# Kernel tuning notes

Hardware: AMD Instinct MI355X
Metric: run time of the kernel (lower is better)

Reference implementation:

```python
import jax, jax.numpy as jnp
import numpy as np

B, L, D, F = 4096, 200, 64, 100000


def setup_inputs() -> dict:
    key = jax.random.key(0)
    ks = jax.random.split(key, 12)
    film_hist = jax.random.randint(ks[0], (B, L), 0, F)                 # padded rated-film indices
    ratings = jax.random.uniform(ks[1], (B, L), jnp.float32) * 4.5 + 0.5  # letterboxd-style 0.5..5
    lengths = jax.random.randint(ks[2], (B,), 1, L + 1)                 # ragged history lengths (>=1)
    film_indices = jax.random.randint(ks[3], (B,), 0, F)                # target films to score
    emb_table = jax.random.normal(ks[4], (F, D), jnp.float32) * 0.1
    W1 = jax.random.normal(ks[5], (5 * D, 2 * D), jnp.float32) * 0.05
    b1 = jnp.zeros((2 * D,), jnp.float32)
    W2 = jax.random.normal(ks[6], (2 * D, D), jnp.float32) * 0.05
    b2 = jnp.zeros((D,), jnp.float32)
    W3 = jax.random.normal(ks[7], (D, 1), jnp.float32) * 0.05
    b3 = jnp.zeros((1,), jnp.float32)
    return {"film_hist": film_hist, "ratings": ratings, "lengths": lengths,
            "film_indices": film_indices, "emb_table": emb_table,
            "W1": W1, "b1": b1, "W2": W2, "b2": b2, "W3": W3, "b3": b3}


def _user_embeddings(film_hist, ratings, lengths, emb_table):
    # mask[b, l] = l < lengths[b]
    mask = jnp.arange(L)[None, :] < lengths[:, None]          # [B, L]
    n = lengths.astype(jnp.float32)                           # [B]
    mean_r = jnp.sum(jnp.where(mask, ratings, 0.0), axis=1) / n
    weights = ratings - mean_r[:, None] + 0.1                 # [B, L]
    hist_emb = emb_table[film_hist]                           # [B, L, D]
    w = hist_emb * weights[:, :, None]                        # weighted film embeddings
    m3 = mask[:, :, None]
    wmin = jnp.min(jnp.where(m3, w, jnp.inf), axis=1)
    wmax = jnp.max(jnp.where(m3, w, -jnp.inf), axis=1)
    wmean = jnp.sum(jnp.where(m3, w, 0.0), axis=1) / n[:, None]
    # median: sort valid entries (pads go to +inf at the end); torch.median
    # returns the lower middle element -> index (n-1)//2
    ws = jnp.sort(jnp.where(m3, w, jnp.inf), axis=1)
    mid = ((lengths - 1) // 2)[:, None, None]                 # [B,1,1]
    wmed = jnp.take_along_axis(ws, jnp.broadcast_to(mid, (B, 1, D)), axis=1)[:, 0, :]
    ue = jnp.concatenate([wmin, wmax, wmean, wmed], axis=1)   # [B, 4D]
    return ue / jnp.linalg.norm(ue, axis=1, keepdims=True)


def reference(film_hist, ratings, lengths, film_indices, emb_table, W1, b1, W2, b2, W3, b3):
    ue = _user_embeddings(film_hist, ratings, lengths, emb_table)  # [B, 4D]
    fe = emb_table[film_indices]                                   # [B, D]
    x = jnp.concatenate([ue, fe], axis=1)                          # [B, 5D]
    h = jax.nn.relu(x @ W1 + b1)   # Dropout(0.2) is identity in eval
    h = jax.nn.relu(h @ W2 + b2)
    return jax.nn.sigmoid(h @ W3 + b3)[:, 0]                       # [B]
```

## Files before the change

### kernel.cpp

```cpp
#include <hip/hip_runtime.h>
#include <hip/hip_bf16.h>
#include <stdint.h>


#define B_ 4096
#define L_ 200
#define D_ 64
#define LPAD 224

__device__ __forceinline__ void xpose_sign(uint32_t (&W)[16]) {
  #define XS(k, jj, m) { uint32_t tt = ((W[k] ^ (W[(k)|(jj)] >> (jj))) & (m)); \
                         W[k] ^= tt; W[(k)|(jj)] ^= (tt << (jj)); }
  XS(0,8,0x00FF00FFu) XS(1,8,0x00FF00FFu) XS(2,8,0x00FF00FFu) XS(3,8,0x00FF00FFu)
  XS(4,8,0x00FF00FFu) XS(5,8,0x00FF00FFu) XS(6,8,0x00FF00FFu) XS(7,8,0x00FF00FFu)
  XS(0,4,0x0F0F0F0Fu) XS(1,4,0x0F0F0F0Fu) XS(2,4,0x0F0F0F0Fu) XS(3,4,0x0F0F0F0Fu)
  XS(8,4,0x0F0F0F0Fu) XS(9,4,0x0F0F0F0Fu) XS(10,4,0x0F0F0F0Fu) XS(11,4,0x0F0F0F0Fu)
  XS(0,2,0x33333333u) XS(1,2,0x33333333u) XS(4,2,0x33333333u) XS(5,2,0x33333333u)
  XS(8,2,0x33333333u) XS(9,2,0x33333333u) XS(12,2,0x33333333u) XS(13,2,0x33333333u)
  XS(0,1,0x55555555u) XS(2,1,0x55555555u) XS(4,1,0x55555555u) XS(6,1,0x55555555u)
  XS(8,1,0x55555555u) XS(10,1,0x55555555u) XS(12,1,0x55555555u) XS(14,1,0x55555555u)
  #undef XS
  const uint32_t S = W[0];
  W[0] = ~S;
  #pragma unroll
  for (int j = 1; j < 16; ++j) W[j] ^= S;
}

template<bool TWO>
__device__ __forceinline__ uint32_t select_med(
    const uint32_t (&W0)[16], const uint32_t (&W1x)[16],
    uint32_t a0, uint32_t a1, int k)
{
  uint32_t prefix = 0;
  #pragma unroll
  for (int bb = 15; bb >= 0; --bb) {
    const uint32_t z0 = a0 & ~W0[15 - bb];
    int cnt = __popc(z0);
    uint32_t z1 = 0u;
    if (TWO) {
      z1 = a1 & ~W1x[15 - bb];
      cnt += __popc(z1);
    }
    cnt += __builtin_amdgcn_update_dpp(0, cnt, 0xB1, 0xF, 0xF, true);
    cnt += __builtin_amdgcn_update_dpp(0, cnt, 0x4E, 0xF, 0xF, true);
    const bool zs = (k < cnt);
    a0 = zs ? z0 : (a0 ^ z0);
    if (TWO) a1 = zs ? z1 : (a1 ^ z1);
    k      = zs ? k : (k - cnt);
    prefix = zs ? prefix : (prefix | (1u << bb));
  }
  return prefix;
}

__global__ __launch_bounds__(256) void stats_kernel(
    const int* __restrict__ film_hist,
    const float* __restrict__ ratings,
    const int* __restrict__ lengths,
    const int* __restrict__ film_indices,
    const float* __restrict__ emb,
    float* __restrict__ x)
{
  __shared__ uint2 pair_s[LPAD];
  __shared__ float red[4];
  __shared__ float ue[4*D_];

  const int t = threadIdx.x;
  const int wv = t >> 6;
  const int lane = t & 63;
  const int d = t >> 2;
  const int sub = t & 3;
  const int b = blockIdx.x;
  const int n = lengths[b];

  const int fi = film_indices[b];
  const float fev = (t < 64) ? emb[(size_t)fi * D_ + t] : 0.f;

  float r = 0.f;
  if (t < LPAD) {
    uint2 e;
    if (t < n) {
      e.x = ((uint32_t)film_hist[(size_t)b*L_ + t]) << 8;
      r = ratings[(size_t)b*L_ + t];
      e.y = __float_as_uint(r);
    } else {
      e.x = 0u; e.y = 0u;
    }
    pair_s[t] = e;
  }
  float s = r;
  #pragma unroll
  for (int off = 32; off; off >>= 1) s += __shfl_down(s, off);
  if (lane == 0) red[wv] = s;
  __syncthreads();
  const float mr1 = 0.1f - (red[0]+red[1]+red[2]+red[3]) / (float)n;

  if (t < n) pair_s[t].y = __float_as_uint(r + mr1);
  __syncthreads();

  const char* eb = (const char*)emb;
  const uint32_t d4 = (uint32_t)d * 4u;
  float vmin = __builtin_inff(), vmax = -__builtin_inff(), vsum = 0.f;
  uint32_t W0[16], W1x[16];
  #pragma unroll
  for (int j = 0; j < 16; ++j) { W0[j] = 0u; W1x[j] = 0u; }

  const int ng    = (n + 15) >> 4;
  const int nfull = n >> 4;

  #define LDSP(G, PE) { \
    _Pragma("unroll") \
    for (int j = 0; j < 4; ++j) PE[j] = pair_s[sub + 16*(G) + 4*j]; }
  #define VMEMG(PE, EV) { \
    _Pragma("unroll") \
    for (int j = 0; j < 4; ++j) \
      EV[j] = *(const float*)(eb + (PE[j].x + d4)); }
  #define CONSG(G, EV, PE) { \
    uint32_t kk[4]; \
    _Pragma("unroll") \
    for (int j = 0; j < 4; ++j) { \
      const float w_ = EV[j] * __uint_as_float(PE[j].y); \
      vsum += w_;                       \
      kk[j] = __float_as_uint(w_); \
    } \
    if ((G) < nfull) { \
      _Pragma("unroll") \
      for (int j = 0; j < 4; ++j) { \
        const float w_ = __uint_as_float(kk[j]); \
        vmin = fminf(vmin, w_); vmax = fmaxf(vmax, w_); \
      } \
    } else { \
      _Pragma("unroll") \
      for (int j = 0; j < 4; ++j) { \
        const int l_ = sub + 16*(G) + 4*j; \
        const float w_ = __uint_as_float(kk[j]); \
        vmin = fminf(vmin, (l_ < n) ? w_ :  __builtin_inff()); \
        vmax = fmaxf(vmax, (l_ < n) ? w_ : -__builtin_inff()); \
      } \
    } \
    const uint32_t wA_ = __builtin_amdgcn_perm(kk[1], kk[0], 0x07060302u); \
    const uint32_t wB_ = __builtin_amdgcn_perm(kk[3], kk[2], 0x07060302u); \
    if ((G) < 8) { W0[2*(G)]       = wA_; W0[2*(G)+1]       = wB_; } \
    else         { W1x[2*((G)-8)]  = wA_; W1x[2*((G)-8)+1]  = wB_; } }

  uint2 peA[4], peB[4];
  float evA[4], evB[4];
  LDSP(0, peA); VMEMG(peA, evA);
  #pragma unroll
  for (int gp = 0; gp < 7; ++gp) {
    const int g = 2*gp;
    if (g < ng) {
      if (g+1 < ng) { LDSP(g+1, peB); VMEMG(peB, evB); }
      CONSG(g, evA, peA);
      if (g+2 < ng) { LDSP(g+2, peA); VMEMG(peA, evA); }
      if (g+1 < ng) { CONSG(g+1, evB, peB); }
    }
  }
  #undef LDSP
  #undef VMEMG
  #undef CONSG

  vmin = fminf(vmin, __shfl_xor(vmin, 1));
  vmin = fminf(vmin, __shfl_xor(vmin, 2));
  vmax = fmaxf(vmax, __shfl_xor(vmax, 1));
  vmax = fmaxf(vmax, __shfl_xor(vmax, 2));
  vsum += __shfl_xor(vsum, 1);
  vsum += __shfl_xor(vsum, 2);

  const bool two = (n > 128);
  xpose_sign(W0);
  if (two) xpose_sign(W1x);

  const int cth = (n > sub) ? ((n - sub + 3) >> 2) : 0;
  const int v0 = (cth < 32) ? cth : 32;
  const int v1 = cth - v0;
  const int ce0 = (v0 + 1) >> 1, cf0 = v0 >> 1;
  uint32_t a0 = ((1u << ce0) - 1u) << (16 - ce0);
  if (cf0) a0 |= ((1u << cf0) - 1u) << (32 - cf0);
  const int ce1 = (v1 + 1) >> 1, cf1 = v1 >> 1;
  uint32_t a1 = ((1u << ce1) - 1u) << (16 - ce1);
  if (cf1) a1 |= ((1u << cf1) - 1u) << (32 - cf1);
  if (v1 == 0) a1 = 0u;

  const int k = (n - 1) >> 1;
  const uint32_t prefix = two ? select_med<true >(W0, W1x, a0, a1, k)
                              : select_med<false>(W0, W1x, a0, a1, k);

  if (sub == 0) {
    uint32_t key32 = (prefix << 16) | 0x8000u;
    const float med = (prefix & 0x8000u) ? __uint_as_float(key32 ^ 0x80000000u)
                                         : __uint_as_float(~key32);
    ue[d]       = vmin;
    ue[64 + d]  = vmax;
    ue[128 + d] = vsum / (float)n;
    ue[192 + d] = med;
  }
  __syncthreads();

  const float vv = ue[t];
  float ss = vv * vv;
  #pragma unroll
  for (int off = 32; off; off >>= 1) ss += __shfl_down(ss, off);
  if (lane == 0) red[wv] = ss;
  __syncthreads();
  const float rn = 1.0f / sqrtf(red[0]+red[1]+red[2]+red[3]);

  float* xb = x + (size_t)b * 320;
  xb[t] = vv * rn;
  if (t < 64) xb[256 + t] = fev;
}

#define U_ 8

__global__ __launch_bounds__(256) void mlp_kernel(
    const float* __restrict__ x,
    const float* __restrict__ W1, const float* __restrict__ b1,
    const float* __restrict__ W2, const float* __restrict__ b2,
    const float* __restrict__ W3, const float* __restrict__ b3,
    float* __restrict__ out)
{
  __shared__ float xs[U_*320];
  __shared__ float ph[2048];
  __shared__ float h1s[U_*128];
  __shared__ float h2s[U_*64];
  const int t = threadIdx.x;
  const int u0 = blockIdx.x * U_;

  for (int i = t; i < U_*80; i += 256)
    ((float4*)xs)[i] = ((const float4*)(x + (size_t)u0*320))[i];
  __syncthreads();

  {
    const int j = t & 127, ih = t >> 7;
    const float* Wp = W1 + (size_t)(ih*160)*128 + j;
    const int xo = ih*160;
    float acc[8];
    #pragma unroll
    for (int u = 0; u < U_; ++u) acc[u] = 0.f;
    #pragma unroll 4
    for (int i = 0; i < 160; ++i) {
      const float w = Wp[(size_t)i*128];
      #pragma unroll
      for (int u = 0; u < U_; ++u) acc[u] += xs[u*320 + xo + i] * w;
    }
    #pragma unroll
    for (int u = 0; u < U_; ++u) ph[ih*1024 + u*128 + j] = acc[u];
  }
  __syncthreads();
  for (int e = t; e < 1024; e += 256) {
    h1s[e] = fmaxf(b1[e & 127] + ph[e] + ph[1024 + e], 0.f);
  }
  __syncthreads();

  {
    const int j2 = t & 63, ih2 = t >> 6;
    const float* Wp = W2 + (size_t)(ih2*32)*64 + j2;
    const int ho = ih2*32;
    float acc[8];
    #pragma unroll
    for (int u = 0; u < U_; ++u) acc[u] = 0.f;
    #pragma unroll 4
    for (int i = 0; i < 32; ++i) {
      const float w = Wp[(size_t)i*64];
      #pragma unroll
      for (int u = 0; u < U_; ++u) acc[u] += h1s[u*128 + ho + i] * w;
    }
    #pragma unroll
    for (int u = 0; u < U_; ++u) ph[ih2*512 + u*64 + j2] = acc[u];
  }
  __syncthreads();
  for (int e = t; e < 512; e += 256) {
    h2s[e] = fmaxf(b2[e & 63] + ph[e] + ph[512 + e] + ph[1024 + e] + ph[1536 + e], 0.f);
  }
  __syncthreads();

  {
    const int u = t >> 5, i = t & 31;
    float a = h2s[u*64 + i] * W3[i] + h2s[u*64 + 32 + i] * W3[32 + i];
    #pragma unroll
    for (int off = 16; off; off >>= 1) a += __shfl_xor(a, off);
    if (i == 0) out[u0 + u] = 1.f / (1.f + __expf(-(a + b3[0])));
  }
}

extern "C" void kernel_launch(void* const* d_in, const int* in_sizes, int n_in,
                              void* d_out, int out_size, void* d_ws, size_t ws_size,
                              hipStream_t stream) {
  const int*   film_hist = (const int*)d_in[0];
  const float* ratings   = (const float*)d_in[1];
  const int*   lengths   = (const int*)d_in[2];
  const int*   film_idx  = (const int*)d_in[3];
  const float* emb       = (const float*)d_in[4];
  const float* W1 = (const float*)d_in[5];
  const float* b1 = (const float*)d_in[6];
  const float* W2 = (const float*)d_in[7];
  const float* b2 = (const float*)d_in[8];
  const float* W3 = (const float*)d_in[9];
  const float* b3 = (const float*)d_in[10];

  float* xbuf = (float*)d_ws;
  float* outp = (float*)d_out;

  stats_kernel<<<B_, 256, 0, stream>>>(film_hist, ratings, lengths, film_idx, emb, xbuf);
  mlp_kernel<<<B_/U_, 256, 0, stream>>>(xbuf, W1, b1, W2, b2, W3, b3, outp);
}
```

Measured before the change: 51.49 us.

## Replace shared-memory history staging with per-wave global loads and xor reduction

Drops the LDS staging array of film indices and adjusted ratings along with its two block barriers. Each wave now computes the rating mean with its own strided reads and an xor-shuffle reduction, and the gather loop loads indices and ratings straight from global memory, clamping out-of-range positions. This removes the barriers and LDS traffic. In exchange every wave re-reads the same history row from global or cache, and the index load now sits on the dependent path before each embedding gather, which lengthens that load chain.

New measurement: 61.78 us. 20.0% more time.

```diff
diff --git a/kernel.cpp b/kernel.cpp
--- a/kernel.cpp
+++ b/kernel.cpp
@@ -6,7 +6,6 @@
 #define B_ 4096
 #define L_ 200
 #define D_ 64
-#define LPAD 224
 
 __device__ __forceinline__ void xpose_sign(uint32_t (&W)[16]) {
   #define XS(k, jj, m) { uint32_t tt = ((W[k] ^ (W[(k)|(jj)] >> (jj))) & (m)); \
@@ -60,7 +59,6 @@
     const float* __restrict__ emb,
     float* __restrict__ x)
 {
-  __shared__ uint2 pair_s[LPAD];
   __shared__ float red[4];
   __shared__ float ue[4*D_];
 
@@ -75,27 +73,18 @@
   const int fi = film_indices[b];
   const float fev = (t < 64) ? emb[(size_t)fi * D_ + t] : 0.f;
 
-  float r = 0.f;
-  if (t < LPAD) {
-    uint2 e;
-    if (t < n) {
-      e.x = ((uint32_t)film_hist[(size_t)b*L_ + t]) << 8;
-      r = ratings[(size_t)b*L_ + t];
-      e.y = __float_as_uint(r);
-    } else {
-      e.x = 0u; e.y = 0u;
-    }
-    pair_s[t] = e;
-  }
-  float s = r;
-  #pragma unroll
-  for (int off = 32; off; off >>= 1) s += __shfl_down(s, off);
-  if (lane == 0) red[wv] = s;
-  __syncthreads();
-  const float mr1 = 0.1f - (red[0]+red[1]+red[2]+red[3]) / (float)n;
-
-  if (t < n) pair_s[t].y = __float_as_uint(r + mr1);
-  __syncthreads();
+  const int*   hp = film_hist + (size_t)b * L_;
+  const float* rp = ratings  + (size_t)b * L_;
+
+  float rsum = 0.f;
+  #pragma unroll
+  for (int j = 0; j < 4; ++j) {
+    const int l = lane + 64*j;
+    rsum += (l < n) ? rp[l] : 0.f;
+  }
+  #pragma unroll
+  for (int off = 32; off; off >>= 1) rsum += __shfl_xor(rsum, off);
+  const float mr1 = 0.1f - rsum / (float)n;
 
   const char* eb = (const char*)emb;
   const uint32_t d4 = (uint32_t)d * 4u;
@@ -107,9 +96,23 @@
   const int ng    = (n + 15) >> 4;
   const int nfull = n >> 4;
 
-  #define LDSP(G, PE) { \
-    _Pragma("unroll") \
-    for (int j = 0; j < 4; ++j) PE[j] = pair_s[sub + 16*(G) + 4*j]; }
+  #define GLDP(G, PE) { \
+    if ((G) < nfull) {                        \
+      _Pragma("unroll") \
+      for (int j = 0; j < 4; ++j) { \
+        const int l_ = sub + 16*(G) + 4*j; \
+        PE[j].x = ((uint32_t)hp[l_]) << 8; \
+        PE[j].y = __float_as_uint(rp[l_] + mr1); \
+      } \
+    } else {                                  \
+      _Pragma("unroll") \
+      for (int j = 0; j < 4; ++j) { \
+        const int l_ = sub + 16*(G) + 4*j; \
+        const int li_ = (l_ < n) ? l_ : (n-1); \
+        PE[j].x = ((uint32_t)hp[li_]) << 8; \
+        PE[j].y = (l_ < n) ? __float_as_uint(rp[li_] + mr1) : 0u; \
+      } \
+    } }
   #define VMEMG(PE, EV) { \
     _Pragma("unroll") \
     for (int j = 0; j < 4; ++j) \
@@ -144,18 +147,18 @@
 
   uint2 peA[4], peB[4];
   float evA[4], evB[4];
-  LDSP(0, peA); VMEMG(peA, evA);
+  GLDP(0, peA); VMEMG(peA, evA);
   #pragma unroll
   for (int gp = 0; gp < 7; ++gp) {
     const int g = 2*gp;
     if (g < ng) {
-      if (g+1 < ng) { LDSP(g+1, peB); VMEMG(peB, evB); }
+      if (g+1 < ng) { GLDP(g+1, peB); VMEMG(peB, evB); }
       CONSG(g, evA, peA);
-      if (g+2 < ng) { LDSP(g+2, peA); VMEMG(peA, evA); }
+      if (g+2 < ng) { GLDP(g+2, peA); VMEMG(peA, evA); }
       if (g+1 < ng) { CONSG(g+1, evB, peB); }
     }
   }
-  #undef LDSP
+  #undef GLDP
   #undef VMEMG
   #undef CONSG
 
```
